# Kernel optimization log

Measured on AMD Instinct MI355X. Metric: run time of the kernel, lower is better.

Reference implementation:

```python
import jax, jax.numpy as jnp
import numpy as np

B, C, H, E, K, QT = 256, 1024, 64, 64, 2, 20000

def _mlp(x, W1, b1, W2, b2):
    # GKT MLP (eval mode: dropout off; batch-norm omitted, see notes)
    return jax.nn.relu(jax.nn.relu(x @ W1 + b1) @ W2 + b2)

def setup_inputs() -> dict:
    key = jax.random.key(0)
    ks = jax.random.split(key, 30)
    s = 0.05  # weight scale to keep pre-clamp activations in a sane range
    xt = jax.random.uniform(ks[0], (B,), dtype=jnp.float32)
    qt = jax.random.randint(ks[1], (B,), 0, QT)
    ht = jax.random.normal(ks[2], (B, C, H), dtype=jnp.float32)
    # binary question->concept incidence, ~4 KCs per question, col 0 forced on
    oh = (jax.random.uniform(ks[3], (QT, C)) < 4.0 / C).astype(jnp.float32)
    oh = oh.at[:, 0].set(1.0)
    qt_kc_one_hot = jnp.concatenate([oh, jnp.zeros((1, C), jnp.float32)], axis=0)  # zero padding row
    kc_embeddings = jax.random.normal(ks[4], (C, E), dtype=jnp.float32) * 0.1
    graphs = jax.random.uniform(ks[5], (K, C, C), dtype=jnp.float32)  # graph_model output
    neigh_weight = jnp.float32(0.8)
    MI = H + E
    Ws1 = jax.random.normal(ks[6], (MI, H), jnp.float32) * s; bs1 = jnp.zeros((H,), jnp.float32)
    Ws2 = jax.random.normal(ks[7], (H, H), jnp.float32) * s;  bs2 = jnp.zeros((H,), jnp.float32)
    Wn1 = jax.random.normal(ks[8], (K, 2 * MI, H), jnp.float32) * s; bn1 = jnp.zeros((K, H), jnp.float32)
    Wn2 = jax.random.normal(ks[9], (K, H, H), jnp.float32) * s;      bn2 = jnp.zeros((K, H), jnp.float32)
    ea_w = jax.random.uniform(ks[10], (C,), dtype=jnp.float32)
    We = jax.random.normal(ks[11], (H, H), jnp.float32) * s; be = jnp.zeros((H,), jnp.float32)
    Wa = jax.random.normal(ks[12], (H, H), jnp.float32) * s; ba = jnp.zeros((H,), jnp.float32)
    W_ih = jax.random.normal(ks[13], (H, 3 * H), jnp.float32) * s; b_ih = jnp.zeros((3 * H,), jnp.float32)
    W_hh = jax.random.normal(ks[14], (H, 3 * H), jnp.float32) * s; b_hh = jnp.zeros((3 * H,), jnp.float32)
    Wp = jax.random.normal(ks[15], (H, 1), jnp.float32) * s; bp = jnp.zeros((1,), jnp.float32)
    return dict(xt=xt, qt=qt, ht=ht, qt_kc_one_hot=qt_kc_one_hot, kc_embeddings=kc_embeddings,
                graphs=graphs, neigh_weight=neigh_weight, Ws1=Ws1, bs1=bs1, Ws2=Ws2, bs2=bs2,
                Wn1=Wn1, bn1=bn1, Wn2=Wn2, bn2=bn2, ea_w=ea_w, We=We, be=be, Wa=Wa, ba=ba,
                W_ih=W_ih, b_ih=b_ih, W_hh=W_hh, b_hh=b_hh, Wp=Wp, bp=bp)

def reference(xt, qt, ht, qt_kc_one_hot, kc_embeddings, graphs, neigh_weight,
              Ws1, bs1, Ws2, bs2, Wn1, bn1, Wn2, bn2, ea_w, We, be, Wa, ba,
              W_ih, b_ih, W_hh, b_hh, Wp, bp):
    # ---- _aggregate: the fusion loops never write back, so tmp_ht = cat(ht, kc_emb)
    mask = qt_kc_one_hot[qt]                                   # [B, C] gather of binary incidence
    kc = jnp.broadcast_to(kc_embeddings[None], (mask.shape[0], C, E))
    tmp_ht = jnp.concatenate([ht, kc], axis=-1)                # [B, C, H+E]
    # ---- _agg_neighbors
    self_ht = tmp_ht * mask[..., None]
    self_feat = jnp.clip(_mlp(self_ht, Ws1, bs1, Ws2, bs2), -10.0, 10.0)
    neigh_ht = jnp.clip(jnp.concatenate([self_ht, tmp_ht], axis=-1), -5.0, 5.0)  # [B,C,2(H+E)]
    # bug-faithful adj: mean of graphs[k] rows over sample 0's active concepts
    a0 = mask[0]                                               # [C]
    denom = jnp.maximum(a0.sum(), 1.0)
    adj = jnp.clip(jnp.einsum('c,kcd->kd', a0, graphs) / denom, -5.0, 5.0)       # [K, C]
    nb = jax.vmap(lambda W1, b1, W2, b2: _mlp(neigh_ht, W1, b1, W2, b2))(Wn1, bn1, Wn2, bn2)
    nb = jnp.clip(nb, -5.0, 5.0)                               # [K, B, C, H]
    w = jnp.clip(neigh_weight, 0.1, 0.9)
    nf = jnp.clip(adj[0][None, :, None] * nb[0], -5.0, 5.0)
    for k in range(1, K):
        nf = jnp.clip(w * nf + (1.0 - w) * adj[k][None, :, None] * nb[k], -5.0, 5.0)
    m_next = jnp.clip(jnp.where(mask[..., None] > 0.5, self_feat, nf), -50.0, 50.0)
    # ---- erase-add gate
    g = ea_w[None, :, None]
    res = m_next - g * jax.nn.sigmoid(m_next @ We + be) * m_next + g * jnp.tanh(m_next @ Wa + ba)
    # ---- GRUCell over flattened (B*C) rows
    gi = res @ W_ih + b_ih
    gh = ht @ W_hh + b_hh
    ir, iz, in_ = jnp.split(gi, 3, axis=-1)
    hr, hz, hn = jnp.split(gh, 3, axis=-1)
    r = jax.nn.sigmoid(ir + hr)
    z = jax.nn.sigmoid(iz + hz)
    n = jnp.tanh(in_ + r * hn)
    h_next = (1.0 - z) * n + z * ht                            # [B, C, H]
    y = jax.nn.sigmoid(h_next @ Wp + bp)[..., 0]               # [B, C]
    return y
```

## Files before the change

### kernel.cpp

```cpp
#include <hip/hip_runtime.h>

#define DEVINL __device__ __forceinline__

typedef __bf16 bf16x8 __attribute__((ext_vector_type(8)));
typedef float  f32x4  __attribute__((ext_vector_type(4)));
typedef unsigned u32x2 __attribute__((ext_vector_type(2)));

static constexpr size_t kAdjOff  = 0;
static constexpr size_t kBiasOff = 8192;
static constexpr size_t kFragOff = 8192 + 786432;

static constexpr int FB_Wn1h0 = 0,  FB_Wn1h1 = 8,  FB_Wn2_0 = 16, FB_Wn2_1 = 24;
static constexpr int FB_Ws1h  = 32, FB_Ws2   = 40, FB_We    = 48, FB_Wa    = 56;
static constexpr int FB_Wih   = 64, FB_Whh   = 88;

DEVINL unsigned short bf16r(float f) {
  unsigned u = __builtin_bit_cast(unsigned, f);
  unsigned r = ((u >> 16) & 1u) + 0x7FFFu;
  return (unsigned short)((u + r) >> 16);
}
DEVINL float sigmoidf_(float x) { return __builtin_amdgcn_rcpf(1.f + __expf(-x)); }
DEVINL float tanhf_(float x)    { return 1.f - 2.f * __builtin_amdgcn_rcpf(1.f + __expf(2.f * x)); }

DEVINL unsigned pkbf(float a, float b) {
  unsigned d;
  asm("v_cvt_pk_bf16_f32 %0, %1, %2" : "=v"(d) : "v"(a), "v"(b));
  return d;
}

DEVINL f32x4 mfma16(bf16x8 a, bf16x8 b, f32x4 c) {
  return __builtin_amdgcn_mfma_f32_16x16x32_bf16(a, b, c, 0, 0, 0);
}

DEVINL unsigned clip2_(unsigned x) {
  float lo = __builtin_bit_cast(float, x << 16);
  float hi = __builtin_bit_cast(float, x & 0xFFFF0000u);
  lo = fminf(fmaxf(lo, -5.f), 5.f);
  hi = fminf(fmaxf(hi, -5.f), 5.f);
  return (__builtin_bit_cast(unsigned, lo) >> 16) | (__builtin_bit_cast(unsigned, hi) & 0xFFFF0000u);
}
DEVINL bf16x8 clip5(bf16x8 a) {
  uint4 u = __builtin_bit_cast(uint4, a);
  u.x = clip2_(u.x); u.y = clip2_(u.y); u.z = clip2_(u.z); u.w = clip2_(u.w);
  return __builtin_bit_cast(bf16x8, u);
}

DEVINL void dsw64(unsigned addr, unsigned long long d) {
  asm volatile("ds_write_b64 %0, %1" :: "v"(addr), "v"(d));
}
DEVINL void ldA2_tr(unsigned addr, bf16x8& a0, bf16x8& a1) {
  u32x2 r0, r1, r2, r3;
  asm volatile(
      "ds_read_b64_tr_b16 %0, %4\n\t"
      "ds_read_b64_tr_b16 %1, %4 offset:512\n\t"
      "ds_read_b64_tr_b16 %2, %4 offset:1024\n\t"
      "ds_read_b64_tr_b16 %3, %4 offset:1536\n\t"
      "s_waitcnt lgkmcnt(0)"
      : "=&v"(r0), "=&v"(r1), "=&v"(r2), "=&v"(r3)
      : "v"(addr));
  uint4 u0{r0.x, r0.y, r1.x, r1.y};
  uint4 u1{r2.x, r2.y, r3.x, r3.y};
  a0 = __builtin_bit_cast(bf16x8, u0);
  a1 = __builtin_bit_cast(bf16x8, u1);
}

__global__ void prep_adj_kernel(const int* __restrict__ qt, const float* __restrict__ onehot,
                                const float* __restrict__ graphs, float* __restrict__ adjw) {
  __shared__ float a0v[1024];
  __shared__ int   aidx[1024];
  __shared__ int   s_nnz;
  __shared__ float s_den;
  const int tid = threadIdx.x;
  const int k = blockIdx.x >> 2, chunk = blockIdx.x & 3;
  if (tid == 0) { s_nnz = 0; s_den = 0.f; }
  __syncthreads();
  const int q0 = qt[0];
  float lsum = 0.f;
#pragma unroll
  for (int i = 0; i < 4; i++) {
    int c = tid * 4 + i;
    float v = onehot[(size_t)q0 * 1024 + c];
    lsum += v;
    if (v != 0.f) { int p = atomicAdd(&s_nnz, 1); aidx[p] = c; a0v[p] = v; }
  }
#pragma unroll
  for (int off = 32; off >= 1; off >>= 1) lsum += __shfl_xor(lsum, off, 64);
  if ((tid & 63) == 0) atomicAdd(&s_den, lsum);
  __syncthreads();
  const float denom = fmaxf(s_den, 1.f);
  const int nnz = s_nnz;
  const int d = chunk * 256 + tid;
  const float* G = graphs + (size_t)k * 1048576 + d;
  float sum = 0.f;
  for (int j = 0; j < nnz; j++) sum += a0v[j] * G[(size_t)aidx[j] * 1024];
  adjw[k * 1024 + d] = fminf(fmaxf(sum / denom, -5.f), 5.f);
}

__global__ void prep_bias_kernel(const float* __restrict__ kc, const float* __restrict__ Wn1,
                                 const float* __restrict__ bn1, const float* __restrict__ Ws1,
                                 const float* __restrict__ bs1, float* __restrict__ biasTab) {
  int gid = blockIdx.x * 256 + threadIdx.x;
  int j = gid & 63;
  int c = (gid >> 6) & 1023;
  int tab = gid >> 16;
  const float* kcr = kc + (size_t)c * 64;
  float s;
  if (tab < 2) {
    s = bn1[tab * 64 + j];
    const float* W = Wn1 + ((size_t)tab * 256 + 192) * 64 + j;
#pragma unroll 4
    for (int e = 0; e < 64; e++) s += fminf(fmaxf(kcr[e], -5.f), 5.f) * W[(size_t)e * 64];
  } else {
    s = bs1[j];
    const float* W = Ws1 + (size_t)64 * 64 + j;
#pragma unroll 4
    for (int e = 0; e < 64; e++) s += kcr[e] * W[(size_t)e * 64];
  }
  int c16 = c >> 4, rr = c & 3, qq = (c & 15) >> 2, nt = j >> 4;
  int lane = qq * 16 + (j & 15);
  biasTab[(size_t)((((c16 * 3 + tab) * 4 + nt) * 64 + lane)) * 4 + rr] = s;
}

__global__ void prep_wfrag_kernel(const float* __restrict__ Wn1, const float* __restrict__ Wn2,
                                  const float* __restrict__ Ws1, const float* __restrict__ Ws2,
                                  const float* __restrict__ We,  const float* __restrict__ Wa,
                                  const float* __restrict__ Wih, const float* __restrict__ Whh,
                                  uint4* __restrict__ wfrag) {
  const int bid = blockIdx.x, lane = threadIdx.x;
  int mat, ks, nt;
  if (bid < 64) { mat = bid >> 3; ks = (bid >> 2) & 1; nt = bid & 3; }
  else { int f2 = bid - 64; mat = 8 + f2 / 24; int f = f2 % 24; ks = f / 12; nt = f % 12; }
  const float* base = Wn1; int stride = 64;
  switch (mat) {
    case 0: base = Wn1 + (size_t)128 * 64; break;
    case 1: base = Wn1 + (size_t)(256 + 128) * 64; break;
    case 2: base = Wn2; break;
    case 3: base = Wn2 + (size_t)64 * 64; break;
    case 4: base = Ws1; break;
    case 5: base = Ws2; break;
    case 6: base = We; break;
    case 7: base = Wa; break;
    case 8: base = Wih; stride = 192; break;
    case 9: base = Whh; stride = 192; break;
  }
  const int qq = lane >> 4, col = nt * 16 + (lane & 15);
  union { unsigned short u[8]; uint4 v; } tmp;
#pragma unroll
  for (int jj = 0; jj < 8; jj++) {
    int k = ks * 32 + ((jj < 4) ? (qq * 4 + jj) : (16 + qq * 4 + (jj - 4)));
    tmp.u[jj] = bf16r(base[(size_t)k * stride + col]);
  }
  wfrag[(size_t)bid * 64 + lane] = tmp.v;
}

__global__ __launch_bounds__(256, 2) void gkt_main_kernel(
    const int* __restrict__ qt, const float* __restrict__ onehot, const float* __restrict__ ht,
    const float* __restrict__ nw, const float* __restrict__ bn2, const float* __restrict__ be,
    const float* __restrict__ ba, const float* __restrict__ bih, const float* __restrict__ bhh,
    const float* __restrict__ Wp, const float* __restrict__ bp, const float* __restrict__ eaw,
    const float* __restrict__ bs2, const float* __restrict__ adjw, const float* __restrict__ biasTab,
    const bf16x8* __restrict__ wfrag, float* __restrict__ out) {
  __shared__ __align__(128) unsigned short hbuf[4][2][64][16];
  __shared__ __align__(16) float tokp[4][2][64];
  __shared__ __align__(16) uint4 gfrag[40 * 64];

  const int tid = threadIdx.x;
  const int wv = tid >> 6, lane = tid & 63;
  const int q = lane >> 4, cl = lane & 15;
  const int t0 = (blockIdx.x * 4 + wv) * 32;
  const int b = t0 >> 10, c0 = t0 & 1023, c16 = c0 >> 4;

  const unsigned hbA = (unsigned)(size_t)&hbuf[wv][0][0][0] + lane * 8;
  const unsigned hbB = hbA + 2048;
  const unsigned pbA = (unsigned)(size_t)&hbuf[wv][0][0][0] + cl * 32 + q * 8;
  const unsigned pbB = pbA + 2048;
  float* tpA = &tokp[wv][0][0];
  float* tpB = &tokp[wv][1][0];

  {
    const uint4* wf4 = (const uint4*)wfrag;
#pragma unroll
    for (int i = 0; i < 10; i++) {
      int f = wv * 10 + i;
      gfrag[f * 64 + lane] = wf4[(64 + f) * 64 + lane];
    }
  }

  if (lane < 32) {
    const int s = lane >> 4, l = lane & 15;
    const int c = c0 + lane;
    float* tp = &tokp[wv][s][0];
    tp[l]      = onehot[(size_t)qt[b] * 1024 + c];
    tp[16 + l] = adjw[c];
    tp[32 + l] = adjw[1024 + c];
    tp[48 + l] = eaw[c];
  }
  {
    const float4* ht4 = (const float4*)ht;
#pragma unroll
    for (int i = 0; i < 8; i++) {
      float4 v = ht4[(size_t)t0 * 16 + i * 64 + lane];
      int e = i * 64 + lane;
      int tok = e >> 4, s = tok >> 4, tk = tok & 15, fb = (e & 15) * 4;
      hbuf[wv][s][fb + 0][tk] = bf16r(v.x);
      hbuf[wv][s][fb + 1][tk] = bf16r(v.y);
      hbuf[wv][s][fb + 2][tk] = bf16r(v.z);
      hbuf[wv][s][fb + 3][tk] = bf16r(v.w);
    }
  }

  auto ldB = [&](int frag) -> bf16x8 { return wfrag[frag * 64 + lane]; };
  auto ldG = [&](int fr) -> bf16x8 {
    return (fr < 40) ? *(const bf16x8*)&gfrag[fr * 64 + lane]
                     : wfrag[(64 + fr) * 64 + lane];
  };
  auto ldTP4 = [&](const float* tp, int base) -> f32x4 {
    return *(const f32x4*)(tp + base + q * 4);
  };
  auto packRow = [&](unsigned pb, int nt, float v0, float v1, float v2, float v3) {
    unsigned long long d = (unsigned long long)pkbf(v0, v1) |
                           ((unsigned long long)pkbf(v2, v3) << 32);
    dsw64(pb + nt * 512, d);
  };
  const f32x4* bt4 = (const f32x4*)biasTab;

  bf16x8 fX[8], fY[8];
#pragma unroll
  for (int i = 0; i < 8; i++) fX[i] = ldB(FB_Wn1h0 + i);

  __syncthreads();

  const float wmix = fminf(fmaxf(nw[0], 0.1f), 0.9f);

  bf16x8 xrA[2], xrB[2];
  ldA2_tr(hbA, xrA[0], xrA[1]);
  ldA2_tr(hbB, xrB[0], xrB[1]);
  bf16x8 xcA[2], xcB[2];
#pragma unroll
  for (int ks = 0; ks < 2; ks++) { xcA[ks] = clip5(xrA[ks]); xcB[ks] = clip5(xrB[ks]); }

  f32x4 nfA[4], nfB[4];

#pragma unroll
  for (int k2 = 0; k2 < 2; k2++) {
#pragma unroll
    for (int i = 0; i < 8; i++) fY[i] = ldB((k2 ? FB_Wn2_1 : FB_Wn2_0) + i);
    f32x4 acA[4], acB[4];
#pragma unroll
    for (int nt = 0; nt < 4; nt++) {
      acA[nt] = bt4[((c16 * 3 + k2) * 4 + nt) * 64 + lane];
      acB[nt] = bt4[(((c16 + 1) * 3 + k2) * 4 + nt) * 64 + lane];
    }
#pragma unroll
    for (int ks = 0; ks < 2; ks++)
#pragma unroll
      for (int nt = 0; nt < 4; nt++) {
        acA[nt] = mfma16(xcA[ks], fX[ks * 4 + nt], acA[nt]);
        acB[nt] = mfma16(xcB[ks], fX[ks * 4 + nt], acB[nt]);
      }
#pragma unroll
    for (int nt = 0; nt < 4; nt++)
      packRow(pbA, nt, fmaxf(acA[nt][0], 0.f), fmaxf(acA[nt][1], 0.f),
                       fmaxf(acA[nt][2], 0.f), fmaxf(acA[nt][3], 0.f));
#pragma unroll
    for (int nt = 0; nt < 4; nt++)
      packRow(pbB, nt, fmaxf(acB[nt][0], 0.f), fmaxf(acB[nt][1], 0.f),
                       fmaxf(acB[nt][2], 0.f), fmaxf(acB[nt][3], 0.f));

#pragma unroll
    for (int i = 0; i < 8; i++) fX[i] = ldB((k2 ? FB_Ws1h : FB_Wn1h1) + i);
    bf16x8 a0, a1;
    f32x4 c2A[4], c2B[4];
#pragma unroll
    for (int nt = 0; nt < 4; nt++) {
      float bz = bn2[k2 * 64 + nt * 16 + cl];
      c2A[nt] = {bz, bz, bz, bz};
      c2B[nt] = c2A[nt];
    }
    ldA2_tr(hbA, a0, a1);
#pragma unroll
    for (int nt = 0; nt < 4; nt++) {
      c2A[nt] = mfma16(a0, fY[nt], c2A[nt]);
      c2A[nt] = mfma16(a1, fY[4 + nt], c2A[nt]);
    }
    ldA2_tr(hbB, a0, a1);
#pragma unroll
    for (int nt = 0; nt < 4; nt++) {
      c2B[nt] = mfma16(a0, fY[nt], c2B[nt]);
      c2B[nt] = mfma16(a1, fY[4 + nt], c2B[nt]);
    }
    {
      f32x4 avA = ldTP4(tpA, (1 + k2) * 16), avB = ldTP4(tpB, (1 + k2) * 16);
#pragma unroll
      for (int nt = 0; nt < 4; nt++)
#pragma unroll
        for (int r = 0; r < 4; r++) {
          float nbA = fminf(fmaxf(c2A[nt][r], 0.f), 5.f);
          float nbB = fminf(fmaxf(c2B[nt][r], 0.f), 5.f);
          float vA = avA[r] * nbA, vB = avB[r] * nbB;
          if (k2 == 0) {
            nfA[nt][r] = wmix * fminf(fmaxf(vA, -5.f), 5.f);
            nfB[nt][r] = wmix * fminf(fmaxf(vB, -5.f), 5.f);
          } else {
            nfA[nt][r] = fminf(fmaxf(nfA[nt][r] + (1.f - wmix) * vA, -5.f), 5.f);
            nfB[nt][r] = fminf(fmaxf(nfB[nt][r] + (1.f - wmix) * vB, -5.f), 5.f);
          }
        }
    }
  }

  bool anySelf = __any((lane < 32) && (tokp[wv][lane >> 4][lane & 15] > 0.5f));
  if (anySelf) {
#pragma unroll
    for (int i = 0; i < 8; i++) fY[i] = ldB(FB_Ws2 + i);
    f32x4 acA[4], acB[4];
#pragma unroll
    for (int nt = 0; nt < 4; nt++) {
      acA[nt] = bt4[((c16 * 3 + 2) * 4 + nt) * 64 + lane];
      acB[nt] = bt4[(((c16 + 1) * 3 + 2) * 4 + nt) * 64 + lane];
    }
#pragma unroll
    for (int ks = 0; ks < 2; ks++)
#pragma unroll
      for (int nt = 0; nt < 4; nt++) {
        acA[nt] = mfma16(xrA[ks], fX[ks * 4 + nt], acA[nt]);
        acB[nt] = mfma16(xrB[ks], fX[ks * 4 + nt], acB[nt]);
      }
#pragma unroll
    for (int nt = 0; nt < 4; nt++)
      packRow(pbA, nt, fmaxf(acA[nt][0], 0.f), fmaxf(acA[nt][1], 0.f),
                       fmaxf(acA[nt][2], 0.f), fmaxf(acA[nt][3], 0.f));
#pragma unroll
    for (int nt = 0; nt < 4; nt++)
      packRow(pbB, nt, fmaxf(acB[nt][0], 0.f), fmaxf(acB[nt][1], 0.f),
                       fmaxf(acB[nt][2], 0.f), fmaxf(acB[nt][3], 0.f));
    bf16x8 a0, a1;
    f32x4 c2A[4], c2B[4];
#pragma unroll
    for (int nt = 0; nt < 4; nt++) {
      float bz = bs2[nt * 16 + cl];
      c2A[nt] = {bz, bz, bz, bz};
      c2B[nt] = c2A[nt];
    }
    ldA2_tr(hbA, a0, a1);
#pragma unroll
    for (int nt = 0; nt < 4; nt++) {
      c2A[nt] = mfma16(a0, fY[nt], c2A[nt]);
      c2A[nt] = mfma16(a1, fY[4 + nt], c2A[nt]);
    }
    ldA2_tr(hbB, a0, a1);
#pragma unroll
    for (int nt = 0; nt < 4; nt++) {
      c2B[nt] = mfma16(a0, fY[nt], c2B[nt]);
      c2B[nt] = mfma16(a1, fY[4 + nt], c2B[nt]);
    }
    {
      f32x4 mkA = ldTP4(tpA, 0), mkB = ldTP4(tpB, 0);
#pragma unroll
      for (int nt = 0; nt < 4; nt++)
#pragma unroll
        for (int r = 0; r < 4; r++) {
          float sfA = fminf(fmaxf(c2A[nt][r], 0.f), 10.f);
          float sfB = fminf(fmaxf(c2B[nt][r], 0.f), 10.f);
          nfA[nt][r] = (mkA[r] > 0.5f) ? sfA : nfA[nt][r];
          nfB[nt][r] = (mkB[r] > 0.5f) ? sfB : nfB[nt][r];
        }
    }
  }

#pragma unroll
  for (int i = 0; i < 8; i++) fX[i] = ldB(FB_We + i);
#pragma unroll
  for (int nt = 0; nt < 4; nt++) packRow(pbA, nt, nfA[nt][0], nfA[nt][1], nfA[nt][2], nfA[nt][3]);
#pragma unroll
  for (int nt = 0; nt < 4; nt++) packRow(pbB, nt, nfB[nt][0], nfB[nt][1], nfB[nt][2], nfB[nt][3]);
  bf16x8 mfA[2], mfB[2];
  ldA2_tr(hbA, mfA[0], mfA[1]);
  ldA2_tr(hbB, mfB[0], mfB[1]);
  {
#pragma unroll
    for (int i = 0; i < 8; i++) fY[i] = ldB(FB_Wa + i);
    f32x4 eA[4], eB[4];
#pragma unroll
    for (int nt = 0; nt < 4; nt++) {
      float bz = be[nt * 16 + cl];
      eA[nt] = {bz, bz, bz, bz};
      eB[nt] = eA[nt];
    }
#pragma unroll
    for (int ks = 0; ks < 2; ks++)
#pragma unroll
      for (int nt = 0; nt < 4; nt++) {
        eA[nt] = mfma16(mfA[ks], fX[ks * 4 + nt], eA[nt]);
        eB[nt] = mfma16(mfB[ks], fX[ks * 4 + nt], eB[nt]);
      }
    {
      f32x4 gvA = ldTP4(tpA, 48), gvB = ldTP4(tpB, 48);
#pragma unroll
      for (int nt = 0; nt < 4; nt++)
#pragma unroll
        for (int r = 0; r < 4; r++) {
          float mA = nfA[nt][r], mB = nfB[nt][r];
          nfA[nt][r] = mA - gvA[r] * sigmoidf_(eA[nt][r]) * mA;
          nfB[nt][r] = mB - gvB[r] * sigmoidf_(eB[nt][r]) * mB;
        }
    }
    f32x4 aA[4], aB[4];
#pragma unroll
    for (int nt = 0; nt < 4; nt++) {
      float bz = ba[nt * 16 + cl];
      aA[nt] = {bz, bz, bz, bz};
      aB[nt] = aA[nt];
    }
#pragma unroll
    for (int ks = 0; ks < 2; ks++)
#pragma unroll
      for (int nt = 0; nt < 4; nt++) {
        aA[nt] = mfma16(mfA[ks], fY[ks * 4 + nt], aA[nt]);
        aB[nt] = mfma16(mfB[ks], fY[ks * 4 + nt], aB[nt]);
      }
    {
      f32x4 gvA = ldTP4(tpA, 48), gvB = ldTP4(tpB, 48);
#pragma unroll
      for (int nt = 0; nt < 4; nt++)
#pragma unroll
        for (int r = 0; r < 4; r++) {
          nfA[nt][r] += gvA[r] * tanhf_(aA[nt][r]);
          nfB[nt][r] += gvB[r] * tanhf_(aB[nt][r]);
        }
    }
  }

#pragma unroll
  for (int nt = 0; nt < 4; nt++) packRow(pbA, nt, nfA[nt][0], nfA[nt][1], nfA[nt][2], nfA[nt][3]);
#pragma unroll
  for (int nt = 0; nt < 4; nt++) packRow(pbB, nt, nfB[nt][0], nfB[nt][1], nfB[nt][2], nfB[nt][3]);
  bf16x8 rfA[2], rfB[2];
  ldA2_tr(hbA, rfA[0], rfA[1]);
  ldA2_tr(hbB, rfB[0], rfB[1]);

  float brz[4], bzz[4], bnn[4], bhn[4], wp4[4];
#pragma unroll
  for (int nt = 0; nt < 4; nt++) {
    int col = nt * 16 + cl;
    brz[nt] = bih[col] + bhh[col];
    bzz[nt] = bih[64 + col] + bhh[64 + col];
    bnn[nt] = bih[128 + col];
    bhn[nt] = bhh[128 + col];
    wp4[nt] = Wp[col];
  }
  const float bpv = bp[0];

  auto gruStream = [&](const bf16x8* rf, const bf16x8* xr, int tbase) {
    float htv[16];
#pragma unroll
    for (int nt = 0; nt < 4; nt++)
#pragma unroll
      for (int r = 0; r < 4; r++)
        htv[nt * 4 + r] = ht[(size_t)(t0 + tbase + q * 4 + r) * 64 + nt * 16 + cl];

    f32x4 gR[4], gZ[4], gN[4], gH[4];
#pragma unroll
    for (int nt = 0; nt < 4; nt++) {
      gR[nt] = {brz[nt], brz[nt], brz[nt], brz[nt]};
      gZ[nt] = {bzz[nt], bzz[nt], bzz[nt], bzz[nt]};
      gN[nt] = {bnn[nt], bnn[nt], bnn[nt], bnn[nt]};
      gH[nt] = {bhn[nt], bhn[nt], bhn[nt], bhn[nt]};
    }
#pragma unroll
    for (int ks = 0; ks < 2; ks++)
#pragma unroll
      for (int nt = 0; nt < 4; nt++) {
        bf16x8 bi_r = ldG(ks * 12 + nt);
        bf16x8 bh_r = ldG(24 + ks * 12 + nt);
        bf16x8 bi_z = ldG(ks * 12 + 4 + nt);
        bf16x8 bh_z = ldG(24 + ks * 12 + 4 + nt);
        bf16x8 bi_n = ldG(ks * 12 + 8 + nt);
        bf16x8 bh_n = ldG(24 + ks * 12 + 8 + nt);
        gR[nt] = mfma16(rf[ks], bi_r, gR[nt]);
        gR[nt] = mfma16(xr[ks], bh_r, gR[nt]);
        gZ[nt] = mfma16(rf[ks], bi_z, gZ[nt]);
        gZ[nt] = mfma16(xr[ks], bh_z, gZ[nt]);
        gN[nt] = mfma16(rf[ks], bi_n, gN[nt]);
        gH[nt] = mfma16(xr[ks], bh_n, gH[nt]);
      }

#pragma unroll
    for (int r = 0; r < 4; r++) {
      int tok = tbase + q * 4 + r;
      float part = 0.f;
#pragma unroll
      for (int nt = 0; nt < 4; nt++) {
        float rr = sigmoidf_(gR[nt][r]);
        float zz = sigmoidf_(gZ[nt][r]);
        float nval = tanhf_(gN[nt][r] + rr * gH[nt][r]);
        float hnx = (1.f - zz) * nval + zz * htv[nt * 4 + r];
        part += hnx * wp4[nt];
      }
      part += __shfl_xor(part, 1, 64);
      part += __shfl_xor(part, 2, 64);
      part += __shfl_xor(part, 4, 64);
      part += __shfl_xor(part, 8, 64);
      if (cl == 0) out[t0 + tok] = sigmoidf_(part + bpv);
    }
  };
  gruStream(rfA, xrA, 0);
  gruStream(rfB, xrB, 16);
}

extern "C" void kernel_launch(void* const* d_in, const int* in_sizes, int n_in,
                              void* d_out, int out_size, void* d_ws, size_t ws_size,
                              hipStream_t stream) {
  const int*   qt     = (const int*)d_in[1];
  const float* ht     = (const float*)d_in[2];
  const float* onehot = (const float*)d_in[3];
  const float* kc     = (const float*)d_in[4];
  const float* graphs = (const float*)d_in[5];
  const float* nw     = (const float*)d_in[6];
  const float* Ws1    = (const float*)d_in[7];
  const float* bs1    = (const float*)d_in[8];
  const float* Ws2    = (const float*)d_in[9];
  const float* bs2    = (const float*)d_in[10];
  const float* Wn1    = (const float*)d_in[11];
  const float* bn1    = (const float*)d_in[12];
  const float* Wn2    = (const float*)d_in[13];
  const float* bn2    = (const float*)d_in[14];
  const float* eaw    = (const float*)d_in[15];
  const float* We     = (const float*)d_in[16];
  const float* be     = (const float*)d_in[17];
  const float* Wa     = (const float*)d_in[18];
  const float* ba     = (const float*)d_in[19];
  const float* Wih    = (const float*)d_in[20];
  const float* bih    = (const float*)d_in[21];
  const float* Whh    = (const float*)d_in[22];
  const float* bhh    = (const float*)d_in[23];
  const float* Wp     = (const float*)d_in[24];
  const float* bp     = (const float*)d_in[25];
  float* out = (float*)d_out;

  float* adjw    = (float*)((char*)d_ws + kAdjOff);
  float* biasTab = (float*)((char*)d_ws + kBiasOff);
  uint4* wfragU  = (uint4*)((char*)d_ws + kFragOff);

  prep_adj_kernel<<<8, 256, 0, stream>>>(qt, onehot, graphs, adjw);
  prep_bias_kernel<<<768, 256, 0, stream>>>(kc, Wn1, bn1, Ws1, bs1, biasTab);
  prep_wfrag_kernel<<<112, 64, 0, stream>>>(Wn1, Wn2, Ws1, Ws2, We, Wa, Wih, Whh, wfragU);
  gkt_main_kernel<<<2048, 256, 0, stream>>>(qt, onehot, ht, nw, bn2, be, ba, bih, bhh,
                                            Wp, bp, eaw, bs2, adjw, biasTab,
                                            (const bf16x8*)wfragU, out);
}
```

Measured before the change: 266.5 us.

## Stage all weight fragments in LDS with 512-thread blocks

Before, only 40 of the 112 weight fragments were staged in shared memory and the rest were read from global memory on every use. Now all 112 fragments (112 KB) are copied into dynamic shared memory, so every B-operand load is an LDS read. To spread that staging cost, blocks grow to 8 waves covering 256 tokens each, with half the grid, and dynamic shared memory is enabled through a function attribute. With about 148 KB of LDS per block, likely only one block fits per CU, which limits occupancy and latency hiding.

```diff
diff --git a/kernel.cpp b/kernel.cpp
--- a/kernel.cpp
+++ b/kernel.cpp
@@ -13,6 +13,11 @@
 static constexpr int FB_Wn1h0 = 0,  FB_Wn1h1 = 8,  FB_Wn2_0 = 16, FB_Wn2_1 = 24;
 static constexpr int FB_Ws1h  = 32, FB_Ws2   = 40, FB_We    = 48, FB_Wa    = 56;
 static constexpr int FB_Wih   = 64, FB_Whh   = 88;
+
+static constexpr unsigned kWldsOff = 0;
+static constexpr unsigned kHbufOff = 114688;
+static constexpr unsigned kTokpOff = 147456;
+static constexpr unsigned kSmemBytes = 151552;
 
 DEVINL unsigned short bf16r(float f) {
   unsigned u = __builtin_bit_cast(unsigned, f);
@@ -153,43 +158,43 @@
   wfrag[(size_t)bid * 64 + lane] = tmp.v;
 }
 
-__global__ __launch_bounds__(256, 2) void gkt_main_kernel(
+__global__ __launch_bounds__(512, 2) void gkt_main_kernel(
     const int* __restrict__ qt, const float* __restrict__ onehot, const float* __restrict__ ht,
     const float* __restrict__ nw, const float* __restrict__ bn2, const float* __restrict__ be,
     const float* __restrict__ ba, const float* __restrict__ bih, const float* __restrict__ bhh,
     const float* __restrict__ Wp, const float* __restrict__ bp, const float* __restrict__ eaw,
     const float* __restrict__ bs2, const float* __restrict__ adjw, const float* __restrict__ biasTab,
     const bf16x8* __restrict__ wfrag, float* __restrict__ out) {
-  __shared__ __align__(128) unsigned short hbuf[4][2][64][16];
-  __shared__ __align__(16) float tokp[4][2][64];
-  __shared__ __align__(16) uint4 gfrag[40 * 64];
+  extern __shared__ __align__(128) char smem[];
 
   const int tid = threadIdx.x;
   const int wv = tid >> 6, lane = tid & 63;
   const int q = lane >> 4, cl = lane & 15;
-  const int t0 = (blockIdx.x * 4 + wv) * 32;
+  const int t0 = (blockIdx.x * 8 + wv) * 32;
   const int b = t0 >> 10, c0 = t0 & 1023, c16 = c0 >> 4;
 
-  const unsigned hbA = (unsigned)(size_t)&hbuf[wv][0][0][0] + lane * 8;
+  const unsigned hbA = kHbufOff + wv * 4096 + lane * 8;
   const unsigned hbB = hbA + 2048;
-  const unsigned pbA = (unsigned)(size_t)&hbuf[wv][0][0][0] + cl * 32 + q * 8;
+  const unsigned pbA = kHbufOff + wv * 4096 + cl * 32 + q * 8;
   const unsigned pbB = pbA + 2048;
-  float* tpA = &tokp[wv][0][0];
-  float* tpB = &tokp[wv][1][0];
+  unsigned short* hbw = (unsigned short*)(smem + kHbufOff) + wv * 2048;
+  float* tpA = (float*)(smem + kTokpOff) + wv * 128;
+  float* tpB = tpA + 64;
 
   {
     const uint4* wf4 = (const uint4*)wfrag;
-#pragma unroll
-    for (int i = 0; i < 10; i++) {
-      int f = wv * 10 + i;
-      gfrag[f * 64 + lane] = wf4[(64 + f) * 64 + lane];
+    uint4* wl = (uint4*)(smem + kWldsOff);
+#pragma unroll
+    for (int i = 0; i < 14; i++) {
+      int f = wv * 14 + i;
+      wl[f * 64 + lane] = wf4[f * 64 + lane];
     }
   }
 
   if (lane < 32) {
     const int s = lane >> 4, l = lane & 15;
     const int c = c0 + lane;
-    float* tp = &tokp[wv][s][0];
+    float* tp = s ? tpB : tpA;
     tp[l]      = onehot[(size_t)qt[b] * 1024 + c];
     tp[16 + l] = adjw[c];
     tp[32 + l] = adjw[1024 + c];
@@ -202,18 +207,18 @@
       float4 v = ht4[(size_t)t0 * 16 + i * 64 + lane];
       int e = i * 64 + lane;
       int tok = e >> 4, s = tok >> 4, tk = tok & 15, fb = (e & 15) * 4;
-      hbuf[wv][s][fb + 0][tk] = bf16r(v.x);
-      hbuf[wv][s][fb + 1][tk] = bf16r(v.y);
-      hbuf[wv][s][fb + 2][tk] = bf16r(v.z);
-      hbuf[wv][s][fb + 3][tk] = bf16r(v.w);
-    }
-  }
-
-  auto ldB = [&](int frag) -> bf16x8 { return wfrag[frag * 64 + lane]; };
-  auto ldG = [&](int fr) -> bf16x8 {
-    return (fr < 40) ? *(const bf16x8*)&gfrag[fr * 64 + lane]
-                     : wfrag[(64 + fr) * 64 + lane];
+      unsigned short* p = hbw + s * 1024 + fb * 16 + tk;
+      p[0]  = bf16r(v.x);
+      p[16] = bf16r(v.y);
+      p[32] = bf16r(v.z);
+      p[48] = bf16r(v.w);
+    }
+  }
+
+  auto ldB = [&](int frag) -> bf16x8 {
+    return *(const bf16x8*)(smem + kWldsOff + frag * 1024 + lane * 16);
   };
+  auto ldG = [&](int fr) -> bf16x8 { return ldB(64 + fr); };
   auto ldTP4 = [&](const float* tp, int base) -> f32x4 {
     return *(const f32x4*)(tp + base + q * 4);
   };
@@ -224,11 +229,11 @@
   };
   const f32x4* bt4 = (const f32x4*)biasTab;
 
+  __syncthreads();
+
   bf16x8 fX[8], fY[8];
 #pragma unroll
   for (int i = 0; i < 8; i++) fX[i] = ldB(FB_Wn1h0 + i);
-
-  __syncthreads();
 
   const float wmix = fminf(fmaxf(nw[0], 0.1f), 0.9f);
 
@@ -309,7 +314,7 @@
     }
   }
 
-  bool anySelf = __any((lane < 32) && (tokp[wv][lane >> 4][lane & 15] > 0.5f));
+  bool anySelf = __any((lane < 32) && ((lane < 16 ? tpA : tpB)[lane & 15] > 0.5f));
   if (anySelf) {
 #pragma unroll
     for (int i = 0; i < 8; i++) fY[i] = ldB(FB_Ws2 + i);
@@ -542,10 +547,17 @@
   float* biasTab = (float*)((char*)d_ws + kBiasOff);
   uint4* wfragU  = (uint4*)((char*)d_ws + kFragOff);
 
+  static bool attrSet = false;
+  if (!attrSet) {
+    hipFuncSetAttribute((const void*)gkt_main_kernel,
+                        hipFuncAttributeMaxDynamicSharedMemorySize, kSmemBytes);
+    attrSet = true;
+  }
+
   prep_adj_kernel<<<8, 256, 0, stream>>>(qt, onehot, graphs, adjw);
   prep_bias_kernel<<<768, 256, 0, stream>>>(kc, Wn1, bn1, Ws1, bs1, biasTab);
   prep_wfrag_kernel<<<112, 64, 0, stream>>>(Wn1, Wn2, Ws1, Ws2, We, Wa, Wih, Whh, wfragU);
-  gkt_main_kernel<<<2048, 256, 0, stream>>>(qt, onehot, ht, nw, bn2, be, ba, bih, bhh,
-                                            Wp, bp, eaw, bs2, adjw, biasTab,
-                                            (const bf16x8*)wfragU, out);
-}
+  gkt_main_kernel<<<1024, 512, kSmemBytes, stream>>>(qt, onehot, ht, nw, bn2, be, ba, bih, bhh,
+                                                     Wp, bp, eaw, bs2, adjw, biasTab,
+                                                     (const bf16x8*)wfragU, out);
+}
```

Measured after the change: 279.3 us. 4.8% more time.
